# Performance work log

Hardware: AMD Instinct MI355X
Metric: run time of the kernel (lower is better)

Reference implementation:

```python
import jax, jax.numpy as jnp
import numpy as np

B, S, D = 8, 4096, 1024
G, V = 2, 320
TAU = 1.0
EPS = 1e-7


def setup_inputs() -> dict:
    key = jax.random.key(0)
    k_x, k_w, k_cb, k_u = jax.random.split(key, 4)
    x = jax.random.normal(k_x, (B, S, D), dtype=jnp.float32)
    W = jax.random.normal(k_w, (D, G * V), dtype=jnp.float32) * (1.0 / np.sqrt(D))
    b = jnp.zeros((G * V,), dtype=jnp.float32)
    # nn.init.uniform_ -> U(0,1); codebooks viewed as [G, V, D//G]
    codebooks = jax.random.uniform(k_cb, (G, V, D // G), dtype=jnp.float32)
    # standard Gumbel(0,1) noise, one per logit: shape [B*S*G, V]
    u = jax.random.uniform(k_u, (B * S * G, V), dtype=jnp.float32,
                           minval=1e-6, maxval=1.0 - 1e-6)
    gumbel = -jnp.log(-jnp.log(u))
    return {"x": x, "W": W, "b": b, "codebooks": codebooks, "gumbel": gumbel}


def reference(x, W, b, codebooks, gumbel):
    Bx, Sx, Dx = x.shape
    Gx, Vx, _ = codebooks.shape
    N = Bx * Sx
    # logit projection: [B,S,D] @ [D, G*V] -> flatten to [N*G, V]
    logits = (jnp.einsum('bsd,de->bse', x, W) + b).reshape(N * Gx, Vx)
    # gumbel-softmax, hard=True with straight-through estimator
    y_soft = jax.nn.softmax((logits + gumbel) / TAU, axis=-1)
    idx = jnp.argmax(y_soft, axis=-1)
    y_hard = jax.nn.one_hot(idx, Vx, dtype=y_soft.dtype)
    one_hot_st = y_hard + y_soft - jax.lax.stop_gradient(y_soft)  # fwd == y_hard
    # codebook lookup via (mostly one-hot) contraction: [N,G,V] x [G,V,d] -> [N,G,d]
    q = jnp.einsum('ngv,gvd->ngd', one_hot_st.reshape(N, Gx, Vx), codebooks)
    quantized = q.reshape(Bx, Sx, Dx)
    # perplexity from clean (non-gumbel) softmax probs
    probs = jax.nn.softmax(logits.reshape(N, Gx, Vx), axis=-1)
    avg_probs = probs.mean(axis=0)  # [G, V]
    perplexity = jnp.exp(-jnp.sum(avg_probs * jnp.log(avg_probs + EPS), axis=-1)).mean()
    return (quantized, perplexity)
```

## Files before the change

### kernel.cpp

```cpp
#include <hip/hip_runtime.h>
#include <hip/hip_bf16.h>
#include <math.h>

#define NROWS 32768
#define DD    1024
#define EE    640
#define VV    320
#define BM    128
#define KT    32
#define CTN   40

typedef __attribute__((ext_vector_type(8))) short short8;
typedef __attribute__((ext_vector_type(4))) short short4v;
typedef __attribute__((ext_vector_type(4))) float float4v;

static __device__ __forceinline__ unsigned short f2bf(float f) {
    unsigned int u = __float_as_uint(f);
    return (unsigned short)((u + 0x7fffu + ((u >> 16) & 1u)) >> 16);
}

static __device__ __forceinline__ void gload_lds16(const void* g, void* l) {
    __builtin_amdgcn_global_load_lds(
        (const __attribute__((address_space(1))) unsigned int*)g,
        (__attribute__((address_space(3))) unsigned int*)l, 16, 0, 0);
}

__global__ void pack_w(const float* __restrict__ W, unsigned short* __restrict__ bp)
{
    const int t = threadIdx.x;
    const int tile = blockIdx.x * 4 + (t >> 6);
    const int lane = t & 63;
    const int kt = tile / CTN, ct = tile % CTN;
    const int k0 = kt * 32 + (lane >> 4) * 8;
    const int col = ct * 16 + (lane & 15);
    unsigned short v1[8];
    #pragma unroll
    for (int e = 0; e < 8; ++e)
        v1[e] = f2bf(W[(size_t)(k0 + e) * EE + col]);
    *(short8*)(bp + ((size_t)tile * 64 + lane) * 8) = *(const short8*)v1;
}

__global__ __launch_bounds__(1024, 4) void fused_mfma(
    const float* __restrict__ x, const unsigned short* __restrict__ bp,
    const float* __restrict__ bias, const float* __restrict__ cb,
    const float* __restrict__ gum, float* __restrict__ out,
    float* __restrict__ probs_acc)
{
    __shared__ unsigned short Bs[2][32 * EE];
    __shared__ unsigned short As[2][BM * 32];
    __shared__ float probs_blk[EE];
    __shared__ float pmax[8][BM];
    __shared__ float psum[8][BM];
    __shared__ int   pidx[8][BM];
    __shared__ int   fidx[BM][2];
    __shared__ float finv[BM][2];

    const int t    = threadIdx.x;
    const int lane = t & 63;
    const int w    = t >> 6;
    const int rg   = w >> 3;
    const int cg   = w & 7;
    const int n0   = blockIdx.x * BM;

    float4v acc[4][5];
    #pragma unroll
    for (int rf = 0; rf < 4; ++rf)
        #pragma unroll
        for (int ct = 0; ct < 5; ++ct)
            acc[rf][ct] = (float4v)0.f;

    const int r0 = t >> 3, kq0 = t & 7;
    const int abase = (r0 >> 4)*512 + ((r0 & 15) + ((kq0 >> 1) << 4))*8 + ((kq0 & 1) << 2);
    const float* xr = x + (size_t)(n0 + r0) * DD + kq0 * 4;

    auto writeA = [&](int bb, float4 v) {
        short4v s1;
        s1[0] = (short)f2bf(v.x); s1[1] = (short)f2bf(v.y);
        s1[2] = (short)f2bf(v.z); s1[3] = (short)f2bf(v.w);
        *(short4v*)&As[bb][abase] = s1;
    };
    auto stageB = [&](int bb, int kt) {
        const unsigned short* src = bp + (size_t)kt * (32 * EE);
        gload_lds16(src + (size_t)t * 8,          &Bs[bb][t * 8]);
        gload_lds16(src + (size_t)(t + 1024) * 8, &Bs[bb][(t + 1024) * 8]);
        if (t < 512)
            gload_lds16(src + (size_t)(t + 2048) * 8, &Bs[bb][(t + 2048) * 8]);
    };

    float4 pA = *(const float4*)(xr);
    stageB(0, 0);
    __syncthreads();
    writeA(0, pA);
    __syncthreads();

    int cur = 0;
    for (int kt = 0; kt < KT; ++kt) {
        const bool more = (kt + 1 < KT);
        if (more) {
            stageB(cur ^ 1, kt + 1);
            pA = *(const float4*)(xr + (kt + 1) * 32);
        }
        short8 af[4];
        #pragma unroll
        for (int rf = 0; rf < 4; ++rf)
            af[rf] = *(const short8*)&As[cur][(rg*4 + rf)*512 + lane*8];
        #pragma unroll
        for (int ct = 0; ct < 5; ++ct) {
            short8 bf = *(const short8*)&Bs[cur][((cg*5 + ct)*64 + lane)*8];
            #pragma unroll
            for (int rf = 0; rf < 4; ++rf)
                acc[rf][ct] = __builtin_amdgcn_mfma_f32_16x16x32_bf16(af[rf], bf, acc[rf][ct], 0, 0, 0);
        }
        if (more) writeA(cur ^ 1, pA);
        __syncthreads();
        cur ^= 1;
    }

    {
        float bv[5];
        #pragma unroll
        for (int ct = 0; ct < 5; ++ct) bv[ct] = bias[cg*80 + ct*16 + (lane & 15)];
        #pragma unroll
        for (int rf = 0; rf < 4; ++rf)
            #pragma unroll
            for (int ct = 0; ct < 5; ++ct) {
                acc[rf][ct][0] += bv[ct]; acc[rf][ct][1] += bv[ct];
                acc[rf][ct][2] += bv[ct]; acc[rf][ct][3] += bv[ct];
            }
    }

    const int g = cg >> 2;
    const int goff0 = (cg & 3)*80 + (lane & 15);
    #pragma unroll
    for (int rf = 0; rf < 4; ++rf) {
        #pragma unroll
        for (int r = 0; r < 4; ++r) {
            const int rowA = rg*64 + rf*16 + ((lane >> 4) << 2) + r;
            const float* grow = gum + ((size_t)(n0 + rowA)*2 + g)*VV + goff0;
            float m1 = -1e30f; int bi = 0; float es = 0.f;
            #pragma unroll
            for (int ct = 0; ct < 5; ++ct) {
                float z  = acc[rf][ct][r];
                float zg = z + grow[ct*16];
                if (zg > m1) { m1 = zg; bi = goff0 + ct*16; }
                es += __expf(z);
            }
            #pragma unroll
            for (int off = 1; off < 16; off <<= 1) {
                float om = __shfl_xor(m1, off);
                int   ob = __shfl_xor(bi, off);
                if (om > m1 || (om == m1 && ob < bi)) { m1 = om; bi = ob; }
                es += __shfl_xor(es, off);
            }
            if ((lane & 15) == 0) {
                pmax[cg][rowA] = m1; pidx[cg][rowA] = bi; psum[cg][rowA] = es;
            }
        }
    }
    for (int c = t; c < EE; c += 1024) probs_blk[c] = 0.f;
    __syncthreads();

    if (t < 256) {
        const int row = t & 127, gg = t >> 7;
        float m1 = -1e30f; int bi = 0x7fffffff; float s = 0.f;
        #pragma unroll
        for (int c = 0; c < 4; ++c) {
            const float om = pmax[gg*4 + c][row];
            const int   ob = pidx[gg*4 + c][row];
            if (om > m1 || (om == m1 && ob < bi)) { m1 = om; bi = ob; }
            s += psum[gg*4 + c][row];
        }
        fidx[row][gg] = bi;
        finv[row][gg] = 1.f / s;
    }
    __syncthreads();

    float pacc[5];
    #pragma unroll
    for (int ct = 0; ct < 5; ++ct) pacc[ct] = 0.f;
    #pragma unroll
    for (int rf = 0; rf < 4; ++rf) {
        #pragma unroll
        for (int r = 0; r < 4; ++r) {
            const int rowA = rg*64 + rf*16 + ((lane >> 4) << 2) + r;
            const float inv = finv[rowA][g];
            #pragma unroll
            for (int ct = 0; ct < 5; ++ct)
                pacc[ct] += __expf(acc[rf][ct][r]) * inv;
        }
    }
    #pragma unroll
    for (int off = 16; off < 64; off <<= 1)
        #pragma unroll
        for (int ct = 0; ct < 5; ++ct)
            pacc[ct] += __shfl_xor(pacc[ct], off);
    if (lane < 16) {
        #pragma unroll
        for (int ct = 0; ct < 5; ++ct)
            atomicAdd(&probs_blk[cg*80 + ct*16 + lane], pacc[ct]);
    }
    __syncthreads();

    for (int c = t; c < EE; c += 1024)
        atomicAdd(&probs_acc[c], probs_blk[c]);

    for (int i = t; i < BM*256; i += 1024) {
        const int row = i >> 8, f4 = i & 255;
        const int gg  = f4 >> 7;
        const int idx = fidx[row][gg];
        const float4 v = *(const float4*)&cb[((size_t)gg*VV + idx)*512 + (size_t)(f4 & 127)*4];
        *(float4*)&out[(size_t)(n0 + row)*DD + (size_t)f4*4] = v;
    }
}

__global__ void perp_kernel(const float* __restrict__ probs_acc,
                            float* __restrict__ outp)
{
    __shared__ float s0[4], s1[4];
    int t = threadIdx.x;
    float p0 = 0.f, p1 = 0.f;
    for (int c = t; c < EE; c += 256) {
        float a = probs_acc[c] * (1.0f / NROWS);
        float v = a * logf(a + 1e-7f);
        if (c < VV) p0 += v; else p1 += v;
    }
    #pragma unroll
    for (int off = 1; off < 64; off <<= 1) {
        p0 += __shfl_xor(p0, off);
        p1 += __shfl_xor(p1, off);
    }
    if ((t & 63) == 0) { s0[t >> 6] = p0; s1[t >> 6] = p1; }
    __syncthreads();
    if (t == 0) {
        float a0 = s0[0] + s0[1] + s0[2] + s0[3];
        float a1 = s1[0] + s1[1] + s1[2] + s1[3];
        outp[0] = 0.5f * (expf(-a0) + expf(-a1));
    }
}

extern "C" void kernel_launch(void* const* d_in, const int* in_sizes, int n_in,
                              void* d_out, int out_size, void* d_ws, size_t ws_size,
                              hipStream_t stream)
{
    const float* x   = (const float*)d_in[0];
    const float* W   = (const float*)d_in[1];
    const float* b   = (const float*)d_in[2];
    const float* cb  = (const float*)d_in[3];
    const float* gum = (const float*)d_in[4];
    float* out = (float*)d_out;

    unsigned short* bp = (unsigned short*)d_ws;
    float* probs_acc = (float*)((char*)d_ws + (size_t)DD*EE*2);

    hipMemsetAsync(probs_acc, 0, EE * sizeof(float), stream);
    pack_w<<<320, 256, 0, stream>>>(W, bp);
    fused_mfma<<<NROWS / BM, 1024, 0, stream>>>(x, bp, b, cb, gum, out, probs_acc);
    perp_kernel<<<1, 256, 0, stream>>>(probs_acc, out + (out_size - 1));
}
```

Baseline: 130.6 us.

## Triple-buffer B tiles and prefetch two K-steps ahead with manual waitcnt

Moves the B-operand LDS staging from double to triple buffering, so global-to-LDS loads for step i+2 are issued while step i computes. Each iteration now uses a single barrier with an explicit partial vmcnt wait, and sched_barrier fences stop the compiler from reordering the loads, MFMAs and A writes. The loop is unrolled by two so the A-register prefetch can ping-pong between two float4 registers. The third B buffer adds about 40KB of LDS, which may reduce occupancy. The hand-written vmcnt(4) count has to match the number of outstanding loads exactly, or the kernel reads stale data.

```diff
diff --git a/kernel.cpp b/kernel.cpp
--- a/kernel.cpp
+++ b/kernel.cpp
@@ -46,7 +46,7 @@
     const float* __restrict__ gum, float* __restrict__ out,
     float* __restrict__ probs_acc)
 {
-    __shared__ unsigned short Bs[2][32 * EE];
+    __shared__ unsigned short Bs[3][32 * EE];
     __shared__ unsigned short As[2][BM * 32];
     __shared__ float probs_blk[EE];
     __shared__ float pmax[8][BM];
@@ -79,41 +79,55 @@
         s1[2] = (short)f2bf(v.z); s1[3] = (short)f2bf(v.w);
         *(short4v*)&As[bb][abase] = s1;
     };
+    const int q0 = t, q1 = t + 1024, q2 = (t < 512) ? t + 2048 : t + 1536;
     auto stageB = [&](int bb, int kt) {
         const unsigned short* src = bp + (size_t)kt * (32 * EE);
-        gload_lds16(src + (size_t)t * 8,          &Bs[bb][t * 8]);
-        gload_lds16(src + (size_t)(t + 1024) * 8, &Bs[bb][(t + 1024) * 8]);
-        if (t < 512)
-            gload_lds16(src + (size_t)(t + 2048) * 8, &Bs[bb][(t + 2048) * 8]);
+        gload_lds16(src + (size_t)q0 * 8, &Bs[bb][q0 * 8]);
+        gload_lds16(src + (size_t)q1 * 8, &Bs[bb][q1 * 8]);
+        gload_lds16(src + (size_t)q2 * 8, &Bs[bb][q2 * 8]);
     };
 
-    float4 pA = *(const float4*)(xr);
-    stageB(0, 0);
-    __syncthreads();
-    writeA(0, pA);
-    __syncthreads();
-
-    int cur = 0;
-    for (int kt = 0; kt < KT; ++kt) {
-        const bool more = (kt + 1 < KT);
-        if (more) {
-            stageB(cur ^ 1, kt + 1);
-            pA = *(const float4*)(xr + (kt + 1) * 32);
-        }
+    auto kbody = [&](int i, int b0, int bstg, float4& curA, float4& nxtA) {
+        asm volatile("s_waitcnt vmcnt(4) lgkmcnt(0)" ::: "memory");
+        __builtin_amdgcn_s_barrier();
+        __builtin_amdgcn_sched_barrier(0);
+        if (i + 2 < KT) {
+            stageB(bstg, i + 2);
+            nxtA = *(const float4*)(xr + (size_t)(i + 2) * 32);
+        }
+        __builtin_amdgcn_sched_barrier(0);
         short8 af[4];
         #pragma unroll
         for (int rf = 0; rf < 4; ++rf)
-            af[rf] = *(const short8*)&As[cur][(rg*4 + rf)*512 + lane*8];
+            af[rf] = *(const short8*)&As[i & 1][(rg*4 + rf)*512 + lane*8];
         #pragma unroll
         for (int ct = 0; ct < 5; ++ct) {
-            short8 bf = *(const short8*)&Bs[cur][((cg*5 + ct)*64 + lane)*8];
+            short8 bf = *(const short8*)&Bs[b0][((cg*5 + ct)*64 + lane)*8];
             #pragma unroll
             for (int rf = 0; rf < 4; ++rf)
                 acc[rf][ct] = __builtin_amdgcn_mfma_f32_16x16x32_bf16(af[rf], bf, acc[rf][ct], 0, 0, 0);
         }
-        if (more) writeA(cur ^ 1, pA);
-        __syncthreads();
-        cur ^= 1;
+        __builtin_amdgcn_sched_barrier(0);
+        if (i + 1 < KT) writeA((i + 1) & 1, curA);
+    };
+
+    float4 pA0, pA1;
+    {
+        stageB(0, 0);
+        float4 a00 = *(const float4*)(xr);
+        stageB(1, 1);
+        pA0 = *(const float4*)(xr + 32);
+        __builtin_amdgcn_sched_barrier(0);
+        writeA(0, a00);
+    }
+
+    int bc = 0;
+    for (int i = 0; i < KT; i += 2) {
+        const int b1 = (bc + 1 > 2) ? 0 : bc + 1;
+        const int b2 = (bc + 2 > 2) ? bc - 1 : bc + 2;
+        kbody(i,     bc, b2, pA0, pA1);
+        kbody(i + 1, b1, bc, pA1, pA0);
+        bc = b2;
     }
 
     {
```

Measured after the change: 128.8 us. Within noise of the previous version (-1.4%).
